# Optimization experiments

Measured on AMD Instinct MI355X. Metric: run time of the kernel, lower is better.

The kernel has to match this reference:

```python
import jax, jax.numpy as jnp
import numpy as np

OUT_H = OUT_W = 7          # cfg.output_size
S = 2                      # fixed samples per bin (static replacement for data-dependent ceil(stride))
G = OUT_H * S              # sampling grid side = 14
SCALES = (0.25, 0.125, 0.0625, 0.03125)   # cfg.pooler_scales for P2..P5
SIZES = (256, 128, 64, 32)                # per-level feature H=W


def _roi_align(feat_p2, feat_p3, feat_p4, feat_p5, proposals):
    # Pad all levels to the largest spatial size and stack -> [4, C, 256, 256].
    # Index clamping below never reads past each level's valid region.
    Hmax = SIZES[0]
    levels = []
    for f, s in zip((feat_p2, feat_p3, feat_p4, feat_p5), SIZES):
        levels.append(jnp.pad(f[0], ((0, 0), (0, Hmax - s), (0, Hmax - s))))
    F = jnp.stack(levels)                      # [4, C, 256, 256]

    N = proposals.shape[0]
    pw = proposals[:, 2] - proposals[:, 0]
    ph = proposals[:, 3] - proposals[:, 1]
    # FPN level assignment: floor(2 + log2(sqrt(area)/224)), clamped to [0,3]
    lvl = jnp.clip(jnp.floor(2.0 + jnp.log2(jnp.sqrt(pw * ph) / 224.0)), 0, 3).astype(jnp.int32)

    sc = jnp.asarray(SCALES, proposals.dtype)[lvl]          # [N]
    box = proposals * sc[:, None]                           # scale to feature coords
    bx1, by1, bx2, by2 = box[:, 0], box[:, 1], box[:, 2], box[:, 3]

    w_stride = (bx2 - bx1) / OUT_W
    h_stride = (by2 - by1) / OUT_H
    w_unit = w_stride / S
    h_unit = h_stride / S

    idx = jnp.arange(G, dtype=proposals.dtype) + 0.5        # sample centers
    xs = bx1[:, None] + idx[None, :] * w_unit[:, None]      # [N, G]
    ys = by1[:, None] + idx[None, :] * h_unit[:, None]      # [N, G]
    x = jnp.broadcast_to(xs[:, None, :], (N, G, G))         # [N, Gy, Gx]
    y = jnp.broadcast_to(ys[:, :, None], (N, G, G))

    # Per-level valid extent for clamping (mirrors feature.shape clamps)
    size_l = jnp.asarray(SIZES, jnp.int32)[lvl][:, None, None]   # [N,1,1]

    x0 = jnp.clip(jnp.floor(x).astype(jnp.int32), 0, size_l - 1)
    x1i = jnp.clip(jnp.floor(x).astype(jnp.int32) + 1, 0, size_l - 1)
    y0 = jnp.clip(jnp.floor(y).astype(jnp.int32), 0, size_l - 1)
    y1i = jnp.clip(jnp.floor(y).astype(jnp.int32) + 1, 0, size_l - 1)

    # Weights use the CLAMPED indices, matching the in-place clamp_ in the original.
    x0f, x1f = x0.astype(x.dtype), x1i.astype(x.dtype)
    y0f, y1f = y0.astype(y.dtype), y1i.astype(y.dtype)
    wa = (x1f - x) * (y1f - y)
    wb = (x1f - x) * (y - y0f)
    wc = (x - x0f) * (y1f - y)
    wd = (x - x0f) * (y - y0f)

    lv = jnp.broadcast_to(lvl[:, None, None], (N, G, G))
    la = F[lv, :, y0, x0]      # [N, G, G, C] gathers (irregular access hotspot)
    lb = F[lv, :, y1i, x0]
    lc = F[lv, :, y0, x1i]
    ld = F[lv, :, y1i, x1i]

    interp = (wa[..., None] * la + wb[..., None] * lb
              + wc[..., None] * lc + wd[..., None] * ld)   # [N, G, G, C]

    C = F.shape[1]
    # Adaptive max pool (7,7): exact SxS blocks since G = 7*S
    pooled = interp.reshape(N, OUT_H, S, OUT_W, S, C).max(axis=(2, 4))  # [N,7,7,C]
    return jnp.transpose(pooled, (0, 3, 1, 2))                          # [N,C,7,7]


def setup_inputs() -> dict:
    key = jax.random.key(0)
    k0, k1, k2, k3, k4 = jax.random.split(key, 5)
    C = 256
    feat_p2 = jax.random.normal(k0, (1, C, 256, 256), jnp.float32)
    feat_p3 = jax.random.normal(k1, (1, C, 128, 128), jnp.float32)
    feat_p4 = jax.random.normal(k2, (1, C, 64, 64), jnp.float32)
    feat_p5 = jax.random.normal(k3, (1, C, 32, 32), jnp.float32)
    N = 512
    u = jax.random.uniform(k4, (N, 4), jnp.float32)
    x1 = u[:, 0] * 700.0
    y1 = u[:, 1] * 700.0
    w = 32.0 + u[:, 2] * 292.0
    h = 32.0 + u[:, 3] * 292.0
    proposals = jnp.stack([x1, y1, x1 + w, y1 + h], axis=1)  # [N,4] image coords
    return {"feat_p2": feat_p2, "feat_p3": feat_p3, "feat_p4": feat_p4,
            "feat_p5": feat_p5, "proposals": proposals}


def reference(feat_p2, feat_p3, feat_p4, feat_p5, proposals):
    return _roi_align(feat_p2, feat_p3, feat_p4, feat_p5, proposals)
```

## Files before the change

### kernel.cpp

```cpp
#include <hip/hip_runtime.h>
#include <hip/hip_bf16.h>
#include <math.h>

#define C_CH 256

__global__ __launch_bounds__(256) void transpose_all(
    const float* __restrict__ f0, const float* __restrict__ f1,
    const float* __restrict__ f2, const float* __restrict__ f3,
    __hip_bfloat16* __restrict__ tf) {
  __shared__ float tile[64][65];
  const int b = blockIdx.x;
  const float* src;
  int S, lg;
  size_t dstoff;
  int sb;
  if (b < 4096) {
    src = f0; S = 65536; lg = 10; dstoff = 0;     sb = b;
  } else if (b < 5120) {
    src = f1; S = 16384; lg = 8;  dstoff = 65536; sb = b - 4096;
  } else if (b < 5376) {
    src = f2; S = 4096;  lg = 6;  dstoff = 81920; sb = b - 5120;
  } else {
    src = f3; S = 1024;  lg = 4;  dstoff = 86016; sb = b - 5376;
  }
  const int nsp_m1 = (1 << lg) - 1;
  const int s0 = (sb & nsp_m1) * 64;
  const int c0 = (sb >> lg) * 64;

  const int t = threadIdx.x;
  {
    const int cl = t >> 4;
    const int sp4 = (t & 15) * 4;
    #pragma unroll
    for (int j = 0; j < 4; ++j) {
      const int c = cl + 16 * j;
      const float4 v = *(const float4*)(src + (size_t)(c0 + c) * S + s0 + sp4);
      tile[c][sp4 + 0] = v.x;
      tile[c][sp4 + 1] = v.y;
      tile[c][sp4 + 2] = v.z;
      tile[c][sp4 + 3] = v.w;
    }
  }
  __syncthreads();
  {
    const int spl = t >> 4;
    const int c4 = (t & 15) * 4;
    __hip_bfloat16* dst = tf + (dstoff + (size_t)s0) * C_CH + c0;
    #pragma unroll
    for (int j = 0; j < 4; ++j) {
      const int sp = spl + 16 * j;
      union { ushort4 u; __hip_bfloat16 h[4]; } p;
      p.h[0] = __float2bfloat16(tile[c4 + 0][sp]);
      p.h[1] = __float2bfloat16(tile[c4 + 1][sp]);
      p.h[2] = __float2bfloat16(tile[c4 + 2][sp]);
      p.h[3] = __float2bfloat16(tile[c4 + 3][sp]);
      *(ushort4*)(dst + (size_t)sp * C_CH + c4) = p.u;
    }
  }
}

__device__ __forceinline__ float bfu(unsigned short s) {
  union { unsigned u; float f; } v;
  v.u = (unsigned)s << 16;
  return v.f;
}

#define OPAD 260

__global__ __launch_bounds__(512) void roi_bf16(
    const unsigned short* __restrict__ tf,
    const float* __restrict__ proposals, float* __restrict__ out) {
  __shared__ int xo0[14], xo1[14], yo0[14], yo1[14];
  __shared__ float wxa[14], wxb[14], wya[14], wyb[14];
  __shared__ float obuf[49 * OPAD];

  const int n = blockIdx.x;
  const int t = threadIdx.x;
  const int lane = t & 63;
  const int w = t >> 6;

  const float px1 = proposals[n * 4 + 0];
  const float py1 = proposals[n * 4 + 1];
  const float px2 = proposals[n * 4 + 2];
  const float py2 = proposals[n * 4 + 3];
  float lt = 2.0f + log2f(sqrtf((px2 - px1) * (py2 - py1)) / 224.0f);
  int lvl = (int)floorf(lt);
  lvl = lvl < 0 ? 0 : (lvl > 3 ? 3 : lvl);

  const float scales[4] = {0.25f, 0.125f, 0.0625f, 0.03125f};
  const int sizes[4] = {256, 128, 64, 32};
  const int offs[4] = {0, 65536, 81920, 86016};
  const float sc = scales[lvl];
  const int sz = sizes[lvl];

  const float bx1 = px1 * sc, by1 = py1 * sc;
  const float w_unit = ((px2 - px1) * sc / 7.0f) * 0.5f;
  const float h_unit = ((py2 - py1) * sc / 7.0f) * 0.5f;

  if (t < 14) {
    const int i = t;
    float x = bx1 + ((float)i + 0.5f) * w_unit;
    int xf = (int)floorf(x);
    int x0 = min(max(xf, 0), sz - 1);
    int x1 = min(max(xf + 1, 0), sz - 1);
    wxa[i] = (float)x1 - x;
    wxb[i] = x - (float)x0;
    xo0[i] = x0 * C_CH;
    xo1[i] = x1 * C_CH;
  } else if (t >= 64 && t < 78) {
    const int i = t - 64;
    float y = by1 + ((float)i + 0.5f) * h_unit;
    int yf = (int)floorf(y);
    int y0 = min(max(yf, 0), sz - 1);
    int y1 = min(max(yf + 1, 0), sz - 1);
    wya[i] = (float)y1 - y;
    wyb[i] = y - (float)y0;
    yo0[i] = y0 * sz * C_CH;
    yo1[i] = y1 * sz * C_CH;
  }
  __syncthreads();

  if (w < 7) {
    const int oh = w;
    const int gy0 = 2 * oh, gy1 = 2 * oh + 1;
    const unsigned short* base = tf + (size_t)offs[lvl] * C_CH + lane * 4;
    const unsigned short* r00 = base + yo0[gy0];
    const unsigned short* r01 = base + yo1[gy0];
    const unsigned short* r10 = base + yo0[gy1];
    const unsigned short* r11 = base + yo1[gy1];
    const float wy0a = wya[gy0], wy0b = wyb[gy0];
    const float wy1a = wya[gy1], wy1b = wyb[gy1];

    float mm[7][4];
    #pragma unroll
    for (int j = 0; j < 7; ++j)
      #pragma unroll
      for (int k = 0; k < 4; ++k) mm[j][k] = -INFINITY;

    #pragma unroll
    for (int gx = 0; gx < 14; ++gx) {
      const int xa = xo0[gx], xb = xo1[gx];
      const ushort4 A0 = *(const ushort4*)(r00 + xa);
      const ushort4 A1 = *(const ushort4*)(r00 + xb);
      const ushort4 B0 = *(const ushort4*)(r01 + xa);
      const ushort4 B1 = *(const ushort4*)(r01 + xb);
      const ushort4 C0 = *(const ushort4*)(r10 + xa);
      const ushort4 C1 = *(const ushort4*)(r10 + xb);
      const ushort4 D0 = *(const ushort4*)(r11 + xa);
      const ushort4 D1 = *(const ushort4*)(r11 + xb);
      const float fa = wxa[gx], fb = wxb[gx];
      const int j = gx >> 1;
      const unsigned short* a0 = (const unsigned short*)&A0;
      const unsigned short* a1 = (const unsigned short*)&A1;
      const unsigned short* b0 = (const unsigned short*)&B0;
      const unsigned short* b1 = (const unsigned short*)&B1;
      const unsigned short* c0 = (const unsigned short*)&C0;
      const unsigned short* c1 = (const unsigned short*)&C1;
      const unsigned short* d0 = (const unsigned short*)&D0;
      const unsigned short* d1 = (const unsigned short*)&D1;
      #pragma unroll
      for (int k = 0; k < 4; ++k) {
        const float h00 = fa * bfu(a0[k]) + fb * bfu(a1[k]);
        const float h01 = fa * bfu(b0[k]) + fb * bfu(b1[k]);
        const float va = wy0a * h00 + wy0b * h01;
        const float h10 = fa * bfu(c0[k]) + fb * bfu(c1[k]);
        const float h11 = fa * bfu(d0[k]) + fb * bfu(d1[k]);
        const float vb = wy1a * h10 + wy1b * h11;
        mm[j][k] = fmaxf(mm[j][k], fmaxf(va, vb));
      }
    }

    #pragma unroll
    for (int ow = 0; ow < 7; ++ow) {
      float4 v = make_float4(mm[ow][0], mm[ow][1], mm[ow][2], mm[ow][3]);
      *(float4*)&obuf[(oh * 7 + ow) * OPAD + lane * 4] = v;
    }
  }
  __syncthreads();

  float* ob = out + (size_t)n * (C_CH * 49);
  for (int i = t; i < C_CH * 49; i += 512) {
    const unsigned c = (unsigned)i / 49u;
    const unsigned p = (unsigned)i - c * 49u;
    ob[i] = obuf[p * OPAD + c];
  }
}

__global__ __launch_bounds__(64) void roi_fallback(
    const float* __restrict__ f0, const float* __restrict__ f1,
    const float* __restrict__ f2, const float* __restrict__ f3,
    const float* __restrict__ proposals, float* __restrict__ out) {
  __shared__ int xo0[14], xo1[14], yo0[14], yo1[14];
  __shared__ float wxa[14], wxb[14], wya[14], wyb[14];
  const int n = blockIdx.x;
  const int cblk = blockIdx.y;
  const int lane = threadIdx.x;
  const int c = cblk * 64 + lane;
  const float px1 = proposals[n * 4 + 0];
  const float py1 = proposals[n * 4 + 1];
  const float px2 = proposals[n * 4 + 2];
  const float py2 = proposals[n * 4 + 3];
  float lt = 2.0f + log2f(sqrtf((px2 - px1) * (py2 - py1)) / 224.0f);
  int lvl = (int)floorf(lt);
  lvl = lvl < 0 ? 0 : (lvl > 3 ? 3 : lvl);
  const float scales[4] = {0.25f, 0.125f, 0.0625f, 0.03125f};
  const int sizes[4] = {256, 128, 64, 32};
  const float sc = scales[lvl];
  const int sz = sizes[lvl];
  const float bx1 = px1 * sc, by1 = py1 * sc;
  const float w_unit = ((px2 - px1) * sc / 7.0f) * 0.5f;
  const float h_unit = ((py2 - py1) * sc / 7.0f) * 0.5f;
  if (lane < 14) {
    float x = bx1 + ((float)lane + 0.5f) * w_unit;
    int xf = (int)floorf(x);
    int x0 = min(max(xf, 0), sz - 1);
    int x1 = min(max(xf + 1, 0), sz - 1);
    wxa[lane] = (float)x1 - x;
    wxb[lane] = x - (float)x0;
    xo0[lane] = x0;
    xo1[lane] = x1;
  } else if (lane >= 32 && lane < 46) {
    const int i = lane - 32;
    float y = by1 + ((float)i + 0.5f) * h_unit;
    int yf = (int)floorf(y);
    int y0 = min(max(yf, 0), sz - 1);
    int y1 = min(max(yf + 1, 0), sz - 1);
    wya[i] = (float)y1 - y;
    wyb[i] = y - (float)y0;
    yo0[i] = y0 * sz;
    yo1[i] = y1 * sz;
  }
  __syncthreads();
  const float* fl = (lvl == 0) ? f0 : (lvl == 1) ? f1 : (lvl == 2) ? f2 : f3;
  const float* base = fl + (size_t)c * sz * sz;
  for (int oh = 0; oh < 7; ++oh) {
    float mm[7];
    #pragma unroll
    for (int ow = 0; ow < 7; ++ow) mm[ow] = -INFINITY;
    #pragma unroll
    for (int sy = 0; sy < 2; ++sy) {
      const int gy = oh * 2 + sy;
      const float* r0 = base + yo0[gy];
      const float* r1 = base + yo1[gy];
      const float wy0 = wya[gy], wy1 = wyb[gy];
      #pragma unroll
      for (int gx = 0; gx < 14; ++gx) {
        float v = wy0 * (wxa[gx] * r0[xo0[gx]] + wxb[gx] * r0[xo1[gx]]) +
                  wy1 * (wxa[gx] * r1[xo0[gx]] + wxb[gx] * r1[xo1[gx]]);
        mm[gx >> 1] = fmaxf(mm[gx >> 1], v);
      }
    }
    #pragma unroll
    for (int ow = 0; ow < 7; ++ow)
      out[((size_t)n * C_CH + c) * 49 + oh * 7 + ow] = mm[ow];
  }
}

extern "C" void kernel_launch(void* const* d_in, const int* in_sizes, int n_in,
                              void* d_out, int out_size, void* d_ws,
                              size_t ws_size, hipStream_t stream) {
  const float* f0 = (const float*)d_in[0];
  const float* f1 = (const float*)d_in[1];
  const float* f2 = (const float*)d_in[2];
  const float* f3 = (const float*)d_in[3];
  const float* props = (const float*)d_in[4];
  float* out = (float*)d_out;
  const int N = in_sizes[4] / 4;

  const size_t needed = (size_t)87040 * C_CH * sizeof(__hip_bfloat16);
  if (ws_size >= needed) {
    __hip_bfloat16* tf = (__hip_bfloat16*)d_ws;
    transpose_all<<<5440, 256, 0, stream>>>(f0, f1, f2, f3, tf);
    roi_bf16<<<N, 512, 0, stream>>>((const unsigned short*)tf, props, out);
  } else {
    roi_fallback<<<dim3(N, 4), 64, 0, stream>>>(f0, f1, f2, f3, props, out);
  }
}
```

Baseline: 144.9 us.

## Split ROI channels across two blocks with register prefetch and swizzled LDS output

After: 141.5 us. -2.3%, faster.

```diff
diff --git a/kernel.cpp b/kernel.cpp
--- a/kernel.cpp
+++ b/kernel.cpp
@@ -65,16 +65,15 @@
   return v.f;
 }
 
-#define OPAD 260
-
-__global__ __launch_bounds__(512) void roi_bf16(
+__global__ __launch_bounds__(512, 8) void roi_bf16(
     const unsigned short* __restrict__ tf,
     const float* __restrict__ proposals, float* __restrict__ out) {
   __shared__ int xo0[14], xo1[14], yo0[14], yo1[14];
   __shared__ float wxa[14], wxb[14], wya[14], wyb[14];
-  __shared__ float obuf[49 * OPAD];
-
-  const int n = blockIdx.x;
+  __shared__ float obuf[49 * 128];
+
+  const int n = blockIdx.x >> 1;
+  const int half = blockIdx.x & 1;
   const int t = threadIdx.x;
   const int lane = t & 63;
   const int w = t >> 6;
@@ -123,7 +122,8 @@
   if (w < 7) {
     const int oh = w;
     const int gy0 = 2 * oh, gy1 = 2 * oh + 1;
-    const unsigned short* base = tf + (size_t)offs[lvl] * C_CH + lane * 4;
+    const unsigned short* base =
+        tf + (size_t)offs[lvl] * C_CH + half * 128 + lane * 2;
     const unsigned short* r00 = base + yo0[gy0];
     const unsigned short* r01 = base + yo1[gy0];
     const unsigned short* r10 = base + yo0[gy1];
@@ -131,23 +131,40 @@
     const float wy0a = wya[gy0], wy0b = wyb[gy0];
     const float wy1a = wya[gy1], wy1b = wyb[gy1];
 
-    float mm[7][4];
-    #pragma unroll
-    for (int j = 0; j < 7; ++j)
-      #pragma unroll
-      for (int k = 0; k < 4; ++k) mm[j][k] = -INFINITY;
-
+    float mm[7][2];
+    #pragma unroll
+    for (int j = 0; j < 7; ++j) {
+      mm[j][0] = -INFINITY;
+      mm[j][1] = -INFINITY;
+    }
+
+    ushort2 nA0, nA1, nB0, nB1, nC0, nC1, nD0, nD1;
+    {
+      const int xa = xo0[0], xb = xo1[0];
+      nA0 = *(const ushort2*)(r00 + xa);
+      nA1 = *(const ushort2*)(r00 + xb);
+      nB0 = *(const ushort2*)(r01 + xa);
+      nB1 = *(const ushort2*)(r01 + xb);
+      nC0 = *(const ushort2*)(r10 + xa);
+      nC1 = *(const ushort2*)(r10 + xb);
+      nD0 = *(const ushort2*)(r11 + xa);
+      nD1 = *(const ushort2*)(r11 + xb);
+    }
     #pragma unroll
     for (int gx = 0; gx < 14; ++gx) {
-      const int xa = xo0[gx], xb = xo1[gx];
-      const ushort4 A0 = *(const ushort4*)(r00 + xa);
-      const ushort4 A1 = *(const ushort4*)(r00 + xb);
-      const ushort4 B0 = *(const ushort4*)(r01 + xa);
-      const ushort4 B1 = *(const ushort4*)(r01 + xb);
-      const ushort4 C0 = *(const ushort4*)(r10 + xa);
-      const ushort4 C1 = *(const ushort4*)(r10 + xb);
-      const ushort4 D0 = *(const ushort4*)(r11 + xa);
-      const ushort4 D1 = *(const ushort4*)(r11 + xb);
+      const ushort2 A0 = nA0, A1 = nA1, B0 = nB0, B1 = nB1;
+      const ushort2 C0 = nC0, C1 = nC1, D0 = nD0, D1 = nD1;
+      if (gx < 13) {
+        const int xa = xo0[gx + 1], xb = xo1[gx + 1];
+        nA0 = *(const ushort2*)(r00 + xa);
+        nA1 = *(const ushort2*)(r00 + xb);
+        nB0 = *(const ushort2*)(r01 + xa);
+        nB1 = *(const ushort2*)(r01 + xb);
+        nC0 = *(const ushort2*)(r10 + xa);
+        nC1 = *(const ushort2*)(r10 + xb);
+        nD0 = *(const ushort2*)(r11 + xa);
+        nD1 = *(const ushort2*)(r11 + xb);
+      }
       const float fa = wxa[gx], fb = wxb[gx];
       const int j = gx >> 1;
       const unsigned short* a0 = (const unsigned short*)&A0;
@@ -159,7 +176,7 @@
       const unsigned short* d0 = (const unsigned short*)&D0;
       const unsigned short* d1 = (const unsigned short*)&D1;
       #pragma unroll
-      for (int k = 0; k < 4; ++k) {
+      for (int k = 0; k < 2; ++k) {
         const float h00 = fa * bfu(a0[k]) + fb * bfu(a1[k]);
         const float h01 = fa * bfu(b0[k]) + fb * bfu(b1[k]);
         const float va = wy0a * h00 + wy0b * h01;
@@ -172,17 +189,19 @@
 
     #pragma unroll
     for (int ow = 0; ow < 7; ++ow) {
-      float4 v = make_float4(mm[ow][0], mm[ow][1], mm[ow][2], mm[ow][3]);
-      *(float4*)&obuf[(oh * 7 + ow) * OPAD + lane * 4] = v;
-    }
-  }
-  __syncthreads();
-
-  float* ob = out + (size_t)n * (C_CH * 49);
-  for (int i = t; i < C_CH * 49; i += 512) {
-    const unsigned c = (unsigned)i / 49u;
-    const unsigned p = (unsigned)i - c * 49u;
-    ob[i] = obuf[p * OPAD + c];
+      const int p = oh * 7 + ow;
+      float2 v = make_float2(mm[ow][0], mm[ow][1]);
+      *(float2*)&obuf[p * 128 + ((lane ^ p) & 63) * 2] = v;
+    }
+  }
+  __syncthreads();
+
+  float* ob = out + (size_t)n * (C_CH * 49) + half * (128 * 49);
+  for (int i = t; i < 128 * 49; i += 512) {
+    const unsigned cl = (unsigned)i / 49u;
+    const unsigned p = (unsigned)i - cl * 49u;
+    const unsigned q = ((cl >> 1) ^ p) & 63u;
+    ob[i] = obuf[p * 128 + q * 2 + (cl & 1)];
   }
 }
 
@@ -271,7 +290,7 @@
   if (ws_size >= needed) {
     __hip_bfloat16* tf = (__hip_bfloat16*)d_ws;
     transpose_all<<<5440, 256, 0, stream>>>(f0, f1, f2, f3, tf);
-    roi_bf16<<<N, 512, 0, stream>>>((const unsigned short*)tf, props, out);
+    roi_bf16<<<2 * N, 512, 0, stream>>>((const unsigned short*)tf, props, out);
   } else {
     roi_fallback<<<dim3(N, 4), 64, 0, stream>>>(f0, f1, f2, f3, props, out);
   }
```
